# Kernel tuning notes

Hardware: AMD Instinct MI355X
Metric: run time of the kernel (lower is better)

## Reference

```python
import jax, jax.numpy as jnp
import numpy as np

EMBED_DIM = 1024
HEAD_SIZE = 128
B, S = 8, 2048

def setup_inputs() -> dict:
    rng = jax.random.key(0)
    k1, k2, k3, k4, k5, k6 = jax.random.split(rng, 6)
    std = 1.0 / EMBED_DIM  # nn.initializers.normal(stddev=1/embed_dim)
    return {
        "key": jax.random.normal(k1, (B, S, EMBED_DIM), dtype=jnp.float32),
        "query": jax.random.normal(k2, (B, S, EMBED_DIM), dtype=jnp.float32),
        "value": jax.random.normal(k3, (B, S, EMBED_DIM), dtype=jnp.float32),
        "W_Q": jax.random.normal(k4, (EMBED_DIM, HEAD_SIZE), dtype=jnp.float32) * std,
        "W_K": jax.random.normal(k5, (EMBED_DIM, HEAD_SIZE), dtype=jnp.float32) * std,
        "W_V": jax.random.normal(k6, (EMBED_DIM, HEAD_SIZE), dtype=jnp.float32) * std,
    }

def reference(key, query, value, W_Q, W_K, W_V):
    # Parallel retention: (Q K^T * causal_mask) V
    q_proj = query @ W_Q        # (B, S, H)
    k_proj = key @ W_K          # (B, S, H)
    v_proj = value @ W_V        # (B, S, H)
    ret = jnp.einsum("bsh,bth->bst", q_proj, k_proj)  # (B, S, S)
    # full_self_retention=False -> lower-triangular (causal) mask
    decay_matrix = jnp.tril(jnp.ones((S, S), dtype=ret.dtype))
    ret = ret * decay_matrix
    return ret @ v_proj          # (B, S, H)
```

## Files before the change

kernel.cpp:

```cpp
#include <hip/hip_runtime.h>
#include <cstdint>

#define B_  8
#define S_  2048
#define E_  1024
#define H_  128
#define NC_ 16

typedef __attribute__((ext_vector_type(8))) short bf16x8;
typedef __attribute__((ext_vector_type(4))) float f32x4;

__device__ __forceinline__ short f2bf(float f){
  uint32_t u = __builtin_bit_cast(uint32_t, f);
  u = (u + 0x7fffu + ((u >> 16) & 1u)) >> 16;
  return (short)u;
}
__device__ __forceinline__ float bf2f(short s){
  uint32_t u = ((uint32_t)(uint16_t)s) << 16;
  return __builtin_bit_cast(float, u);
}

__global__ __launch_bounds__(256) void wt_kernel(
    const float* __restrict__ WQ, const float* __restrict__ WK,
    const float* __restrict__ WV,
    short* __restrict__ WtQ, short* __restrict__ WtK, short* __restrict__ WtV)
{
  int which = blockIdx.z;
  const float* W = which == 0 ? WQ : which == 1 ? WK : WV;
  short* Wt      = which == 0 ? WtQ : which == 1 ? WtK : WtV;
  int k0 = blockIdx.x * 32, n0 = blockIdx.y * 32;
  __shared__ float t[32][33];
  int tx = threadIdx.x & 31, ty = threadIdx.x >> 5;
  #pragma unroll
  for (int i = 0; i < 4; i++)
    t[ty + i * 8][tx] = W[(size_t)(k0 + ty + i * 8) * H_ + n0 + tx];
  __syncthreads();
  #pragma unroll
  for (int i = 0; i < 4; i++)
    Wt[(size_t)(n0 + ty + i * 8) * E_ + k0 + tx] = f2bf(t[tx][ty + i * 8]);
}

__global__ __launch_bounds__(256) void proj_kernel(
    const float* __restrict__ Xq, const float* __restrict__ Xk,
    const float* __restrict__ Xv,
    const short* __restrict__ Wtq, const short* __restrict__ Wtk,
    const short* __restrict__ Wtv,
    short* __restrict__ q, short* __restrict__ k,
    short* __restrict__ kT, short* __restrict__ vT)
{
  int which = blockIdx.y;
  const float* X  = which == 0 ? Xq  : which == 1 ? Xk  : Xv;
  const short* Wt = which == 0 ? Wtq : which == 1 ? Wtk : Wtv;

  int tid = threadIdx.x, lane = tid & 63, wave = tid >> 6;
  int lr = lane & 15, lq = lane >> 4;
  int rowbase = blockIdx.x * 64 + wave * 16;

  __shared__ short Bs[128 * 136];

  const float* xr = X + (size_t)(rowbase + lr) * E_ + lq * 8;

  f32x4 acc[8];
  #pragma unroll
  for (int tn = 0; tn < 8; tn++) acc[tn] = (f32x4){0.f, 0.f, 0.f, 0.f};

  for (int kc = 0; kc < 8; kc++){
    if (kc) __syncthreads();
    #pragma unroll
    for (int v = 0; v < 8; v++){
      int c = v * 256 + tid;
      int n = c >> 4, off = (c & 15) * 8;
      *(bf16x8*)(&Bs[n * 136 + off]) =
          *(const bf16x8*)(Wt + (size_t)n * E_ + kc * 128 + off);
    }
    f32x4 ar[8];
    #pragma unroll
    for (int s = 0; s < 4; s++){
      ar[2 * s]     = *(const f32x4*)(xr + kc * 128 + s * 32);
      ar[2 * s + 1] = *(const f32x4*)(xr + kc * 128 + s * 32 + 4);
    }
    __syncthreads();
    #pragma unroll
    for (int s = 0; s < 4; s++){
      bf16x8 a;
      #pragma unroll
      for (int j = 0; j < 4; j++){
        a[j] = f2bf(ar[2 * s][j]); a[4 + j] = f2bf(ar[2 * s + 1][j]);
      }
      #pragma unroll
      for (int tn = 0; tn < 8; tn++){
        bf16x8 bfr = *(const bf16x8*)(&Bs[(tn * 16 + lr) * 136 + s * 32 + lq * 8]);
        acc[tn] = __builtin_amdgcn_mfma_f32_16x16x32_bf16(a, bfr, acc[tn], 0, 0, 0);
      }
    }
  }

  if (which <= 1){
    short* P = which == 0 ? q : k;
    #pragma unroll
    for (int tn = 0; tn < 8; tn++)
      #pragma unroll
      for (int r4 = 0; r4 < 4; r4++)
        P[(size_t)(rowbase + lq * 4 + r4) * H_ + tn * 16 + lr] = f2bf(acc[tn][r4]);
  }
  if (which >= 1){
    short* T = which == 1 ? kT : vT;
    int b = rowbase >> 11, srow = rowbase & 2047;
    #pragma unroll
    for (int tn = 0; tn < 8; tn++){
      union { short sh[4]; uint2 u; } pk;
      #pragma unroll
      for (int r4 = 0; r4 < 4; r4++) pk.sh[r4] = f2bf(acc[tn][r4]);
      *(uint2*)(T + ((size_t)b * H_ + tn * 16 + lr) * S_ + srow + lq * 4) = pk.u;
    }
  }
}

__global__ __launch_bounds__(256) void chunk_state(
    const short* __restrict__ vT, const short* __restrict__ kT,
    float* __restrict__ M)
{
  int j = blockIdx.x, qtr = blockIdx.y, b = blockIdx.z;
  int tid = threadIdx.x, lane = tid & 63, wave = tid >> 6;
  int wrow = wave * 32;
  int lr = lane & 15, lq = lane >> 4;

  __shared__ short As[128 * 136];
  __shared__ short Bs[32 * 136];

  const short* vtb = vT + (size_t)b * H_ * S_ + j * 128;
  const short* ktb = kT + (size_t)b * H_ * S_ + (size_t)qtr * 32 * S_ + j * 128;

  #pragma unroll
  for (int v = 0; v < 8; v++){
    int c = v * 256 + tid;
    int r = c >> 4, off = (c & 15) * 8;
    *(bf16x8*)(&As[r * 136 + off]) = *(const bf16x8*)(vtb + (size_t)r * S_ + off);
  }
  #pragma unroll
  for (int v = 0; v < 2; v++){
    int c = v * 256 + tid;
    int r = c >> 4, off = (c & 15) * 8;
    *(bf16x8*)(&Bs[r * 136 + off]) = *(const bf16x8*)(ktb + (size_t)r * S_ + off);
  }
  __syncthreads();

  f32x4 acc[2][2];
  #pragma unroll
  for (int a = 0; a < 2; a++)
    #pragma unroll
    for (int c = 0; c < 2; c++) acc[a][c] = (f32x4){0.f, 0.f, 0.f, 0.f};

  #pragma unroll
  for (int s = 0; s < 4; s++){
    int t0 = s * 32;
    bf16x8 af[2], bf[2];
    #pragma unroll
    for (int tm = 0; tm < 2; tm++)
      af[tm] = *(const bf16x8*)(&As[(wrow + tm * 16 + lr) * 136 + t0 + lq * 8]);
    #pragma unroll
    for (int tn = 0; tn < 2; tn++)
      bf[tn] = *(const bf16x8*)(&Bs[(tn * 16 + lr) * 136 + t0 + lq * 8]);
    #pragma unroll
    for (int tm = 0; tm < 2; tm++)
      #pragma unroll
      for (int tn = 0; tn < 2; tn++)
        acc[tm][tn] = __builtin_amdgcn_mfma_f32_16x16x32_bf16(
            af[tm], bf[tn], acc[tm][tn], 0, 0, 0);
  }

  float* mb = M + (size_t)(b * NC_ + j) * 16384;
  #pragma unroll
  for (int tm = 0; tm < 2; tm++)
    #pragma unroll
    for (int tn = 0; tn < 2; tn++)
      #pragma unroll
      for (int r4 = 0; r4 < 4; r4++){
        int row = wrow + tm * 16 + lq * 4 + r4;
        int col = qtr * 32 + tn * 16 + lr;
        mb[row * 128 + col] = acc[tm][tn][r4];
      }
}

__global__ __launch_bounds__(256) void prefix_state(
    const float* __restrict__ M, short* __restrict__ Shi, short* __restrict__ Slo)
{
  int b = blockIdx.y;
  int idx = (blockIdx.x * 256 + threadIdx.x) * 2;
  float2 mv[NC_ - 1];
  #pragma unroll
  for (int j = 0; j < NC_ - 1; j++)
    mv[j] = *(const float2*)(M + (size_t)(b * NC_ + j) * 16384 + idx);

  float r0 = 0.f, r1 = 0.f;
  #pragma unroll
  for (int j = 0; j < NC_; j++){
    size_t o = (size_t)(b * NC_ + j) * 16384 + idx;
    short h0 = f2bf(r0), h1 = f2bf(r1);
    short l0 = f2bf(r0 - bf2f(h0)), l1 = f2bf(r1 - bf2f(h1));
    union { short s[2]; uint32_t u; } ph, pl;
    ph.s[0] = h0; ph.s[1] = h1;
    pl.s[0] = l0; pl.s[1] = l1;
    *(uint32_t*)(Shi + o) = ph.u;
    *(uint32_t*)(Slo + o) = pl.u;
    if (j < NC_ - 1){ r0 += mv[j].x; r1 += mv[j].y; }
  }
}

__global__ __launch_bounds__(256) void passC(
    const short* __restrict__ qb, const short* __restrict__ kb,
    const short* __restrict__ vT, const short* __restrict__ Shi,
    const short* __restrict__ Slo, float* __restrict__ out)
{
  int i = blockIdx.x, qtr = blockIdx.y, b = blockIdx.z;
  int roff = qtr * 32;
  int tid = threadIdx.x, lane = tid & 63, wave = tid >> 6;
  int wcol = wave * 32;
  int lr = lane & 15, lq = lane >> 4;

  __shared__ short Ss[32 * 136];
  __shared__ short Bt0[128 * 136];
  __shared__ short Bt1[128 * 136];

  const short* qbase = qb + ((size_t)b * S_ + i * 128 + roff) * H_;
  const short* kbase = kb + ((size_t)b * S_ + i * 128) * H_;
  const short* vtb   = vT + (size_t)b * H_ * S_ + i * 128;
  const short* shib  = Shi + (size_t)(b * NC_ + i) * 16384;
  const short* slob  = Slo + (size_t)(b * NC_ + i) * 16384;

  bf16x8 kst[8], vst[8], hst[8], lst[8];
  #pragma unroll
  for (int v = 0; v < 8; v++){
    int c = v * 256 + tid;
    int r = c >> 4, off = (c & 15) * 8;
    kst[v] = *(const bf16x8*)(kbase + (size_t)r * H_ + off);
    vst[v] = *(const bf16x8*)(vtb  + (size_t)r * S_ + off);
    hst[v] = *(const bf16x8*)(shib + (size_t)r * 128 + off);
    lst[v] = *(const bf16x8*)(slob + (size_t)r * 128 + off);
  }
  bf16x8 aq[2][4];
  #pragma unroll
  for (int tm = 0; tm < 2; tm++)
    #pragma unroll
    for (int hs = 0; hs < 4; hs++)
      aq[tm][hs] = *(const bf16x8*)(
          qbase + (size_t)(tm * 16 + lr) * H_ + hs * 32 + lq * 8);

  #pragma unroll
  for (int v = 0; v < 8; v++){
    int c = v * 256 + tid;
    int r = c >> 4, off = (c & 15) * 8;
    *(bf16x8*)(&Bt0[r * 136 + off]) = kst[v];
  }
  __syncthreads();

  f32x4 accS[2][2];
  #pragma unroll
  for (int a = 0; a < 2; a++)
    #pragma unroll
    for (int c = 0; c < 2; c++) accS[a][c] = (f32x4){0.f, 0.f, 0.f, 0.f};

  #pragma unroll
  for (int hs = 0; hs < 4; hs++){
    bf16x8 bf[2];
    #pragma unroll
    for (int tn = 0; tn < 2; tn++)
      bf[tn] = *(const bf16x8*)(&Bt0[(wcol + tn * 16 + lr) * 136 + hs * 32 + lq * 8]);
    #pragma unroll
    for (int tm = 0; tm < 2; tm++)
      #pragma unroll
      for (int tn = 0; tn < 2; tn++)
        accS[tm][tn] = __builtin_amdgcn_mfma_f32_16x16x32_bf16(
            aq[tm][hs], bf[tn], accS[tm][tn], 0, 0, 0);
  }

  #pragma unroll
  for (int tm = 0; tm < 2; tm++)
    #pragma unroll
    for (int tn = 0; tn < 2; tn++)
      #pragma unroll
      for (int r4 = 0; r4 < 4; r4++){
        int row = tm * 16 + lq * 4 + r4;
        int col = wcol + tn * 16 + lr;
        float vv = (col <= roff + row) ? accS[tm][tn][r4] : 0.f;
        Ss[row * 136 + col] = f2bf(vv);
      }
  #pragma unroll
  for (int v = 0; v < 8; v++){
    int c = v * 256 + tid;
    int r = c >> 4, off = (c & 15) * 8;
    *(bf16x8*)(&Bt1[r * 136 + off]) = vst[v];
  }
  f32x4 acc[2][2];
  #pragma unroll
  for (int a = 0; a < 2; a++)
    #pragma unroll
    for (int c = 0; c < 2; c++) acc[a][c] = (f32x4){0.f, 0.f, 0.f, 0.f};
  __syncthreads();

  #pragma unroll
  for (int s = 0; s < 4; s++){
    int t0 = s * 32;
    bf16x8 af[2], bf[2];
    #pragma unroll
    for (int tm = 0; tm < 2; tm++)
      af[tm] = *(const bf16x8*)(&Ss[(tm * 16 + lr) * 136 + t0 + lq * 8]);
    #pragma unroll
    for (int tn = 0; tn < 2; tn++)
      bf[tn] = *(const bf16x8*)(&Bt1[(wcol + tn * 16 + lr) * 136 + t0 + lq * 8]);
    #pragma unroll
    for (int tm = 0; tm < 2; tm++)
      #pragma unroll
      for (int tn = 0; tn < 2; tn++)
        acc[tm][tn] = __builtin_amdgcn_mfma_f32_16x16x32_bf16(
            af[tm], bf[tn], acc[tm][tn], 0, 0, 0);
  }
  #pragma unroll
  for (int v = 0; v < 8; v++){
    int c = v * 256 + tid;
    int r = c >> 4, off = (c & 15) * 8;
    *(bf16x8*)(&Bt0[r * 136 + off]) = hst[v];
  }
  __syncthreads();

  #pragma unroll
  for (int hs = 0; hs < 4; hs++){
    bf16x8 bf[2];
    #pragma unroll
    for (int tn = 0; tn < 2; tn++)
      bf[tn] = *(const bf16x8*)(&Bt0[(wcol + tn * 16 + lr) * 136 + hs * 32 + lq * 8]);
    #pragma unroll
    for (int tm = 0; tm < 2; tm++)
      #pragma unroll
      for (int tn = 0; tn < 2; tn++)
        acc[tm][tn] = __builtin_amdgcn_mfma_f32_16x16x32_bf16(
            aq[tm][hs], bf[tn], acc[tm][tn], 0, 0, 0);
  }
  #pragma unroll
  for (int v = 0; v < 8; v++){
    int c = v * 256 + tid;
    int r = c >> 4, off = (c & 15) * 8;
    *(bf16x8*)(&Bt1[r * 136 + off]) = lst[v];
  }
  __syncthreads();

  #pragma unroll
  for (int hs = 0; hs < 4; hs++){
    bf16x8 bf[2];
    #pragma unroll
    for (int tn = 0; tn < 2; tn++)
      bf[tn] = *(const bf16x8*)(&Bt1[(wcol + tn * 16 + lr) * 136 + hs * 32 + lq * 8]);
    #pragma unroll
    for (int tm = 0; tm < 2; tm++)
      #pragma unroll
      for (int tn = 0; tn < 2; tn++)
        acc[tm][tn] = __builtin_amdgcn_mfma_f32_16x16x32_bf16(
            aq[tm][hs], bf[tn], acc[tm][tn], 0, 0, 0);
  }

  float* ob = out + ((size_t)b * S_ + i * 128 + roff) * H_;
  #pragma unroll
  for (int tm = 0; tm < 2; tm++)
    #pragma unroll
    for (int tn = 0; tn < 2; tn++)
      #pragma unroll
      for (int r4 = 0; r4 < 4; r4++){
        int row = tm * 16 + lq * 4 + r4;
        int col = wcol + tn * 16 + lr;
        ob[(size_t)row * H_ + col] = acc[tm][tn][r4];
      }
}

extern "C" void kernel_launch(void* const* d_in, const int* in_sizes, int n_in,
                              void* d_out, int out_size, void* d_ws, size_t ws_size,
                              hipStream_t stream) {
  const float* key   = (const float*)d_in[0];
  const float* query = (const float*)d_in[1];
  const float* value = (const float*)d_in[2];
  const float* WQ    = (const float*)d_in[3];
  const float* WK    = (const float*)d_in[4];
  const float* WV    = (const float*)d_in[5];
  float* out = (float*)d_out;

  char* w = (char*)d_ws;
  short* WtQ = (short*)(w + 0);
  short* WtK = (short*)(w + 262144);
  short* WtV = (short*)(w + 524288);
  size_t o = 786432;
  short* q  = (short*)(w + o); o += 4194304;
  short* k  = (short*)(w + o); o += 4194304;
  short* kT = (short*)(w + o); o += 4194304;
  short* vT = (short*)(w + o); o += 4194304;
  float* M  = (float*)(w + o); o += 8388608;
  short* Shi= (short*)(w + o); o += 4194304;
  short* Slo= (short*)(w + o); o += 4194304;

  wt_kernel   <<<dim3(32, 4, 3),       256, 0, stream>>>(WQ, WK, WV, WtQ, WtK, WtV);
  proj_kernel <<<dim3(256, 3),         256, 0, stream>>>(query, key, value,
                                                         WtQ, WtK, WtV, q, k, kT, vT);
  chunk_state <<<dim3(15, 4, B_),      256, 0, stream>>>(vT, kT, M);
  prefix_state<<<dim3(32, B_),         256, 0, stream>>>(M, Shi, Slo);
  passC       <<<dim3(NC_, 4, B_),     256, 0, stream>>>(q, k, vT, Shi, Slo, out);
}
```

Measured before the change: 232.8 us.

## Fuse chunk-state and prefix-sum kernels into one sequential running-state kernel

Replaces the per-chunk state GEMM kernel and the separate prefix-sum kernel with one kernel. Each block loops over all chunks in order and keeps the running K^T V state in MFMA accumulators. It writes the hi/lo bf16 split of the prefix state directly, which removes the fp32 intermediate buffer M, its global round trip and one kernel launch. The cost is far less parallelism: 64 blocks each run 16 chunks serially, the shared-memory double buffer is not prefetched, and the state is written with narrow 2-byte stores.

```diff
diff --git a/kernel.cpp b/kernel.cpp
--- a/kernel.cpp
+++ b/kernel.cpp
@@ -116,94 +116,68 @@
   }
 }
 
-__global__ __launch_bounds__(256) void chunk_state(
+__global__ __launch_bounds__(256) void fused_state(
     const short* __restrict__ vT, const short* __restrict__ kT,
-    float* __restrict__ M)
+    short* __restrict__ Shi, short* __restrict__ Slo)
 {
-  int j = blockIdx.x, qtr = blockIdx.y, b = blockIdx.z;
+  int rh = blockIdx.x;
+  int ch = blockIdx.y;
+  int b  = blockIdx.z;
   int tid = threadIdx.x, lane = tid & 63, wave = tid >> 6;
-  int wrow = wave * 32;
   int lr = lane & 15, lq = lane >> 4;
 
-  __shared__ short As[128 * 136];
-  __shared__ short Bs[32 * 136];
-
-  const short* vtb = vT + (size_t)b * H_ * S_ + j * 128;
-  const short* ktb = kT + (size_t)b * H_ * S_ + (size_t)qtr * 32 * S_ + j * 128;
-
-  #pragma unroll
-  for (int v = 0; v < 8; v++){
-    int c = v * 256 + tid;
-    int r = c >> 4, off = (c & 15) * 8;
-    *(bf16x8*)(&As[r * 136 + off]) = *(const bf16x8*)(vtb + (size_t)r * S_ + off);
-  }
-  #pragma unroll
-  for (int v = 0; v < 2; v++){
-    int c = v * 256 + tid;
-    int r = c >> 4, off = (c & 15) * 8;
-    *(bf16x8*)(&Bs[r * 136 + off]) = *(const bf16x8*)(ktb + (size_t)r * S_ + off);
-  }
-  __syncthreads();
-
-  f32x4 acc[2][2];
-  #pragma unroll
-  for (int a = 0; a < 2; a++)
-    #pragma unroll
-    for (int c = 0; c < 2; c++) acc[a][c] = (f32x4){0.f, 0.f, 0.f, 0.f};
-
-  #pragma unroll
-  for (int s = 0; s < 4; s++){
-    int t0 = s * 32;
-    bf16x8 af[2], bf[2];
-    #pragma unroll
-    for (int tm = 0; tm < 2; tm++)
-      af[tm] = *(const bf16x8*)(&As[(wrow + tm * 16 + lr) * 136 + t0 + lq * 8]);
-    #pragma unroll
-    for (int tn = 0; tn < 2; tn++)
-      bf[tn] = *(const bf16x8*)(&Bs[(tn * 16 + lr) * 136 + t0 + lq * 8]);
-    #pragma unroll
-    for (int tm = 0; tm < 2; tm++)
-      #pragma unroll
-      for (int tn = 0; tn < 2; tn++)
-        acc[tm][tn] = __builtin_amdgcn_mfma_f32_16x16x32_bf16(
-            af[tm], bf[tn], acc[tm][tn], 0, 0, 0);
-  }
-
-  float* mb = M + (size_t)(b * NC_ + j) * 16384;
-  #pragma unroll
-  for (int tm = 0; tm < 2; tm++)
-    #pragma unroll
-    for (int tn = 0; tn < 2; tn++)
+  __shared__ short As[2][32 * 136];
+  __shared__ short Bs[2][64 * 136];
+
+  const short* vtb = vT + (size_t)b * H_ * S_ + (size_t)(rh * 32) * S_;
+  const short* ktb = kT + (size_t)b * H_ * S_ + (size_t)(ch * 64) * S_;
+
+  f32x4 acc[2];
+  acc[0] = (f32x4){0.f, 0.f, 0.f, 0.f};
+  acc[1] = (f32x4){0.f, 0.f, 0.f, 0.f};
+
+  for (int j = 0; j < NC_; j++){
+    size_t obase = (size_t)(b * NC_ + j) * 16384;
+    #pragma unroll
+    for (int tm = 0; tm < 2; tm++)
       #pragma unroll
       for (int r4 = 0; r4 < 4; r4++){
-        int row = wrow + tm * 16 + lq * 4 + r4;
-        int col = qtr * 32 + tn * 16 + lr;
-        mb[row * 128 + col] = acc[tm][tn][r4];
-      }
-}
-
-__global__ __launch_bounds__(256) void prefix_state(
-    const float* __restrict__ M, short* __restrict__ Shi, short* __restrict__ Slo)
-{
-  int b = blockIdx.y;
-  int idx = (blockIdx.x * 256 + threadIdx.x) * 2;
-  float2 mv[NC_ - 1];
-  #pragma unroll
-  for (int j = 0; j < NC_ - 1; j++)
-    mv[j] = *(const float2*)(M + (size_t)(b * NC_ + j) * 16384 + idx);
-
-  float r0 = 0.f, r1 = 0.f;
-  #pragma unroll
-  for (int j = 0; j < NC_; j++){
-    size_t o = (size_t)(b * NC_ + j) * 16384 + idx;
-    short h0 = f2bf(r0), h1 = f2bf(r1);
-    short l0 = f2bf(r0 - bf2f(h0)), l1 = f2bf(r1 - bf2f(h1));
-    union { short s[2]; uint32_t u; } ph, pl;
-    ph.s[0] = h0; ph.s[1] = h1;
-    pl.s[0] = l0; pl.s[1] = l1;
-    *(uint32_t*)(Shi + o) = ph.u;
-    *(uint32_t*)(Slo + o) = pl.u;
-    if (j < NC_ - 1){ r0 += mv[j].x; r1 += mv[j].y; }
+        int row = rh * 32 + tm * 16 + lq * 4 + r4;
+        int col = ch * 64 + wave * 16 + lr;
+        float v = acc[tm][r4];
+        short h = f2bf(v);
+        Shi[obase + (size_t)row * 128 + col] = h;
+        Slo[obase + (size_t)row * 128 + col] = f2bf(v - bf2f(h));
+      }
+    if (j == NC_ - 1) break;
+
+    int buf = j & 1;
+    #pragma unroll
+    for (int v = 0; v < 2; v++){
+      int c = v * 256 + tid;
+      int r = c >> 4, off = (c & 15) * 8;
+      *(bf16x8*)(&As[buf][r * 136 + off]) =
+          *(const bf16x8*)(vtb + (size_t)r * S_ + j * 128 + off);
+    }
+    #pragma unroll
+    for (int v = 0; v < 4; v++){
+      int c = v * 256 + tid;
+      int r = c >> 4, off = (c & 15) * 8;
+      *(bf16x8*)(&Bs[buf][r * 136 + off]) =
+          *(const bf16x8*)(ktb + (size_t)r * S_ + j * 128 + off);
+    }
+    __syncthreads();
+
+    #pragma unroll
+    for (int s = 0; s < 4; s++){
+      int t0 = s * 32;
+      bf16x8 bfr = *(const bf16x8*)(&Bs[buf][(wave * 16 + lr) * 136 + t0 + lq * 8]);
+      #pragma unroll
+      for (int tm = 0; tm < 2; tm++){
+        bf16x8 af = *(const bf16x8*)(&As[buf][(tm * 16 + lr) * 136 + t0 + lq * 8]);
+        acc[tm] = __builtin_amdgcn_mfma_f32_16x16x32_bf16(af, bfr, acc[tm], 0, 0, 0);
+      }
+    }
   }
 }
 
@@ -391,14 +365,12 @@
   short* k  = (short*)(w + o); o += 4194304;
   short* kT = (short*)(w + o); o += 4194304;
   short* vT = (short*)(w + o); o += 4194304;
-  float* M  = (float*)(w + o); o += 8388608;
   short* Shi= (short*)(w + o); o += 4194304;
   short* Slo= (short*)(w + o); o += 4194304;
 
   wt_kernel   <<<dim3(32, 4, 3),       256, 0, stream>>>(WQ, WK, WV, WtQ, WtK, WtV);
   proj_kernel <<<dim3(256, 3),         256, 0, stream>>>(query, key, value,
                                                          WtQ, WtK, WtV, q, k, kT, vT);
-  chunk_state <<<dim3(15, 4, B_),      256, 0, stream>>>(vT, kT, M);
-  prefix_state<<<dim3(32, B_),         256, 0, stream>>>(M, Shi, Slo);
+  fused_state <<<dim3(4, 2, B_),       256, 0, stream>>>(vT, kT, Shi, Slo);
   passC       <<<dim3(NC_, 4, B_),     256, 0, stream>>>(q, k, vT, Shi, Slo, out);
 }
```

Measured after the change: 237.5 us. +2.0%, slower.
